# Kernel optimization log

Hardware: AMD Instinct MI355X
Metric: run time of the kernel (lower is better)

## Reference

```python
import jax, jax.numpy as jnp
import numpy as np

S = 1024      # seq_len
H = 768       # hidden_size
L = 50        # num_labels
E = 65536     # num_edges
SW = 10       # span_width


def setup_inputs() -> dict:
    key = jax.random.key(0)
    ks = jax.random.split(key, 10)
    hidden_states = jax.random.normal(ks[0], (1, S, H), jnp.float32)
    src = jax.random.randint(ks[1], (E,), 0, S)
    tgt = jax.random.randint(ks[2], (E,), 0, S)
    lbl = jax.random.randint(ks[3], (E,), 0, L)
    edges = jnp.stack([src, tgt, lbl], axis=-1)[None].astype(jnp.int32)  # [1,E,3]
    gcn_W = (jax.random.normal(ks[4], (L, H, H)) * 0.02).astype(jnp.float32)
    gcn_b = jnp.zeros((L, H), jnp.float32)
    attn_w = (jax.random.normal(ks[5], (H,)) * 0.02).astype(jnp.float32)
    attn_b = jnp.zeros((), jnp.float32)
    D = 3 * H
    ms_W1 = (jax.random.normal(ks[6], (D, D)) * 0.02).astype(jnp.float32)
    ms_b1 = jnp.zeros((D,), jnp.float32)
    ms_W2 = (jax.random.normal(ks[7], (D,)) * 0.02).astype(jnp.float32)
    ms_b2 = jnp.zeros((), jnp.float32)
    ant_W = (jax.random.normal(ks[8], (2 * D,)) * 0.02).astype(jnp.float32)
    ant_b = jnp.zeros((), jnp.float32)
    # candidate spans exactly as generate_candidate_spans with span_width=SW
    starts, ends = [], []
    for i in range(S):
        for j in range(i + 1, min(i + SW, S)):
            starts.append(i)
            ends.append(j)
    span_starts = jnp.asarray(np.array(starts, dtype=np.int32))
    span_ends = jnp.asarray(np.array(ends, dtype=np.int32))
    topk = int(S * 0.4)  # seq_lens*0.4 with all-ones attention mask
    return {
        'hidden_states': hidden_states, 'edges': edges,
        'gcn_W': gcn_W, 'gcn_b': gcn_b,
        'attn_w': attn_w, 'attn_b': attn_b,
        'ms_W1': ms_W1, 'ms_b1': ms_b1, 'ms_W2': ms_W2, 'ms_b2': ms_b2,
        'ant_W': ant_W, 'ant_b': ant_b,
        'span_starts': span_starts, 'span_ends': span_ends, 'topk': topk,
    }


def reference(hidden_states, edges, gcn_W, gcn_b, attn_w, attn_b,
              ms_W1, ms_b1, ms_W2, ms_b2, ant_W, ant_b,
              span_starts, span_ends, topk):
    B, Sq, Hd = hidden_states.shape  # B == 1
    nl = gcn_W.shape[0]
    x = hidden_states[0]  # [S,H]

    # ---- GCNLayer: per-label linear + scatter-add + degree norm + relu ----
    src = edges[0, :, 0]
    tgt = edges[0, :, 1]
    lbl = edges[0, :, 2]
    # aggregate source embeddings by (target,label): equivalent to applying
    # W_l per edge then index_add, since the transform is linear per label.
    seg = tgt * nl + lbl                               # [E]
    src_emb = x[src]                                   # [E,H]  gather
    agg = jax.ops.segment_sum(src_emb, seg, num_segments=Sq * nl)
    agg = agg.reshape(Sq, nl, Hd)                      # [S,L,H]
    cnt = jax.ops.segment_sum(jnp.ones_like(seg, jnp.float32), seg,
                              num_segments=Sq * nl).reshape(Sq, nl)
    out = jnp.einsum('slh,lhd->sd', agg, gcn_W) + cnt @ gcn_b  # [S,H]
    degree = jnp.clip(cnt.sum(axis=1), 1.0)[:, None]
    gcn_out = jax.nn.relu(out / degree)

    # combine_strategy == 'add'
    emb = x + gcn_out                                  # [S,H]

    # ---- SpanRepresentation: attention pooling over each span ----
    offs = jnp.arange(SW)                              # span length <= SW
    pos = span_starts[:, None] + offs                  # [N,SW]
    valid = pos <= span_ends[:, None]
    pos_c = jnp.minimum(pos, Sq - 1)
    win = emb[pos_c]                                   # [N,SW,H] gather
    scores = win @ attn_w + attn_b                     # [N,SW]
    scores = jnp.where(valid, scores, -1e9)
    aw = jax.nn.softmax(scores, axis=1)
    attn_out = jnp.einsum('nw,nwh->nh', aw, win)       # [N,H]
    span_vec = jnp.concatenate([emb[span_starts], emb[span_ends], attn_out],
                               axis=-1)                # [N,3H]

    # ---- MentionScorer ----
    hdn = jax.nn.relu(span_vec @ ms_W1 + ms_b1)
    mention_scores = hdn @ ms_W2 + ms_b2               # [N]

    # ---- prune_spans: top-k ----
    topk_scores, topk_idx = jax.lax.top_k(mention_scores, topk)
    pruned = span_vec[topk_idx]                        # [k,3H]

    # ---- antecedent scores: linear over concat pair == sum of two matvecs ----
    D = span_vec.shape[-1]
    s_i = pruned @ ant_W[:D]                           # [k]
    s_j = pruned @ ant_W[D:]                           # [k]
    ant_scores = s_i[:, None] + s_j[None, :] + ant_b   # [k,k]
    # triu mask (antecedent must strictly precede the mention)
    k = pruned.shape[0]
    triu = jnp.triu(jnp.ones((k, k), bool), k=0)
    ant_scores = jnp.where(triu, -1e4, ant_scores)
    dummy = jnp.zeros((k, 1), ant_scores.dtype)
    ant_scores_with_dummy = jnp.concatenate([dummy, ant_scores], axis=1)  # [k,k+1]
    return ant_scores_with_dummy
```

## Files before the change

kernel.cpp:

```cpp
#include <hip/hip_runtime.h>
#include <stdint.h>

typedef __attribute__((ext_vector_type(4))) float f32x4;
typedef __attribute__((ext_vector_type(4))) int i32x4;
typedef __attribute__((ext_vector_type(8))) int i32x8;

#define S_TOK 1024
#define H_DIM 768
#define NLBL  50
#define NEDGE 65536
#define NSEG  (S_TOK * NLBL)
#define NSPAN 9171
#define MPAD  9216
#define DDIM  2304
#define KTOP  409

__device__ __forceinline__ unsigned short f32_to_bf16u(float f) {
  unsigned u = __float_as_uint(f);
  u += 0x7fffu + ((u >> 16) & 1u);
  return (unsigned short)(u >> 16);
}
__device__ __forceinline__ float bf16u_to_f32(unsigned short h) {
  return __uint_as_float(((unsigned)h) << 16);
}
__device__ __forceinline__ unsigned short pack_fp8x2(float a, float b) {
  return (unsigned short)(__builtin_amdgcn_cvt_pk_fp8_f32(a, b, 0, false) & 0xffff);
}
__device__ __forceinline__ unsigned pack_fp8x4(float a, float b, float c, float d) {
  int v = __builtin_amdgcn_cvt_pk_fp8_f32(a, b, 0, false);
  v = __builtin_amdgcn_cvt_pk_fp8_f32(c, d, v, true);
  return (unsigned)v;
}
__device__ __forceinline__ unsigned char pack_fp8x1(float a) {
  return (unsigned char)(__builtin_amdgcn_cvt_pk_fp8_f32(a, a, 0, false) & 0xff);
}

__device__ __forceinline__ void gl_lds16(const void* g, void* l) {
  __builtin_amdgcn_global_load_lds((const __attribute__((address_space(1))) void*)g,
                                   (__attribute__((address_space(3))) void*)l, 16, 0, 0);
}

__global__ __launch_bounds__(256) void convert_fp8(
    const float* __restrict__ in, unsigned* __restrict__ out, int nquads) {
  int i = blockIdx.x * 256 + threadIdx.x;
  if (i >= nquads) return;
  float4 v = ((const float4*)in)[i];
  out[i] = pack_fp8x4(v.x, v.y, v.z, v.w);
}

__global__ __launch_bounds__(256) void transpose_fp8_b(
    const float* __restrict__ in, unsigned char* __restrict__ out, int R, int C) {
  __shared__ float tile[32][33];
  size_t boff = (size_t)blockIdx.z * R * C;
  int tx = threadIdx.x & 31, ty = threadIdx.x >> 5;
  int c0 = blockIdx.x * 32, r0 = blockIdx.y * 32;
#pragma unroll
  for (int i = 0; i < 4; i++)
    tile[ty + 8 * i][tx] = in[boff + (size_t)(r0 + ty + 8 * i) * C + c0 + tx];
  __syncthreads();
#pragma unroll
  for (int i = 0; i < 4; i++)
    out[boff + (size_t)(c0 + ty + 8 * i) * R + r0 + tx] = pack_fp8x1(tile[tx][ty + 8 * i]);
}

__global__ void edge_count2(const int* __restrict__ edges, int* __restrict__ seg_count,
                            int* __restrict__ tgt_count) {
  int e = blockIdx.x * 256 + threadIdx.x;
  if (e >= NEDGE) return;
  int tgt = edges[e * 3 + 1], lbl = edges[e * 3 + 2];
  atomicAdd(&seg_count[tgt * NLBL + lbl], 1);
  atomicAdd(&tgt_count[tgt], 1);
}

__global__ __launch_bounds__(1024) void scan_t(
    const int* __restrict__ cnt, int* __restrict__ offs) {
  __shared__ int part[1024];
  int t = threadIdx.x;
  int c = cnt[t];
  part[t] = c;
  __syncthreads();
  for (int o = 1; o < 1024; o <<= 1) {
    int v = part[t];
    int u = (t >= o) ? part[t - o] : 0;
    __syncthreads();
    part[t] = v + u;
    __syncthreads();
  }
  offs[t] = part[t] - c;
  if (t == 1023) offs[1024] = part[t];
}

__global__ void edge_scatter_t(const int* __restrict__ edges, const int* __restrict__ tgt_off,
                               int* __restrict__ cursor, int* __restrict__ sorted_row) {
  int e = blockIdx.x * 256 + threadIdx.x;
  if (e >= NEDGE) return;
  int src = edges[e * 3], tgt = edges[e * 3 + 1], lbl = edges[e * 3 + 2];
  int pos = tgt_off[tgt] + atomicAdd(&cursor[tgt], 1);
  sorted_row[pos] = lbl * S_TOK + src;
}

template <int EPI>
__global__ __launch_bounds__(256) void gemm_fp8(
    const unsigned char* __restrict__ A, const unsigned char* __restrict__ B,
    unsigned short* __restrict__ Y, float* __restrict__ C,
    const float* __restrict__ b1, const float* __restrict__ w2,
    int M, int Nn, int Kb, int mb, size_t strideB, size_t strideY) {
  __shared__ unsigned char As[128 * 128];
  __shared__ unsigned char Bs[128 * 128];
  int im = blockIdx.x % mb, in_ = blockIdx.x / mb;
  int m0 = im * 128, n0 = in_ * 128;
  const unsigned char* Bl = B + (size_t)blockIdx.y * strideB;

  int t = threadIdx.x;
  int wave = t >> 6, lane = t & 63;
  int wr = wave >> 1, wc = wave & 1;
  int quad = lane >> 4, l15 = lane & 15;
  int lrow = lane >> 3;
  int lk = ((lane & 7) ^ lrow) << 4;

  f32x4 acc[4][4];
  f32x4 zero = {0.f, 0.f, 0.f, 0.f};
#pragma unroll
  for (int mi = 0; mi < 4; mi++)
#pragma unroll
    for (int ni = 0; ni < 4; ni++) acc[mi][ni] = zero;

  for (int kt = 0; kt < Kb; kt += 128) {
#pragma unroll
    for (int i = 0; i < 4; i++) {
      int c = i * 4 + wave;
      int r = c * 8 + lrow;
      gl_lds16(A + (size_t)(m0 + r) * Kb + kt + lk, &As[c * 1024]);
      gl_lds16(Bl + (size_t)(n0 + r) * Kb + kt + lk, &Bs[c * 1024]);
    }
    __syncthreads();
    i32x8 af[4], bg[4];
#pragma unroll
    for (int mi = 0; mi < 4; mi++) {
      int r = wr * 64 + mi * 16 + l15;
      int base = r * 128;
      i32x4 lo = *(const i32x4*)&As[base + (((2 * quad) ^ (r & 7)) << 4)];
      i32x4 hi = *(const i32x4*)&As[base + (((2 * quad + 1) ^ (r & 7)) << 4)];
      af[mi] = __builtin_shufflevector(lo, hi, 0, 1, 2, 3, 4, 5, 6, 7);
    }
#pragma unroll
    for (int ni = 0; ni < 4; ni++) {
      int r = wc * 64 + ni * 16 + l15;
      int base = r * 128;
      i32x4 lo = *(const i32x4*)&Bs[base + (((2 * quad) ^ (r & 7)) << 4)];
      i32x4 hi = *(const i32x4*)&Bs[base + (((2 * quad + 1) ^ (r & 7)) << 4)];
      bg[ni] = __builtin_shufflevector(lo, hi, 0, 1, 2, 3, 4, 5, 6, 7);
    }
#pragma unroll
    for (int mi = 0; mi < 4; mi++)
#pragma unroll
      for (int ni = 0; ni < 4; ni++)
        acc[mi][ni] = __builtin_amdgcn_mfma_scale_f32_16x16x128_f8f6f4(
            af[mi], bg[ni], acc[mi][ni], 0, 0, 0, 0x7f7f7f7f, 0, 0x7f7f7f7f);
    __syncthreads();
  }

  if (EPI == 0) {
    unsigned short* Yl = Y + (size_t)blockIdx.y * strideY;
#pragma unroll
    for (int mi = 0; mi < 4; mi++) {
      int gm = m0 + wr * 64 + mi * 16 + quad * 4;
#pragma unroll
      for (int ni = 0; ni < 4; ni++) {
        int gn = n0 + wc * 64 + ni * 16 + l15;
#pragma unroll
        for (int r = 0; r < 4; r++)
          Yl[(size_t)(gm + r) * Nn + gn] = f32_to_bf16u(acc[mi][ni][r]);
      }
    }
  } else {
    float b1v[4], w2v[4];
#pragma unroll
    for (int ni = 0; ni < 4; ni++) {
      int gn = n0 + wc * 64 + ni * 16 + l15;
      b1v[ni] = b1[gn];
      w2v[ni] = w2[gn];
    }
#pragma unroll
    for (int mi = 0; mi < 4; mi++) {
      int gm = m0 + wr * 64 + mi * 16 + quad * 4;
      float part[4] = {0.f, 0.f, 0.f, 0.f};
#pragma unroll
      for (int ni = 0; ni < 4; ni++)
#pragma unroll
        for (int r = 0; r < 4; r++)
          part[r] += fmaxf(acc[mi][ni][r] + b1v[ni], 0.f) * w2v[ni];
#pragma unroll
      for (int o = 1; o < 16; o <<= 1)
#pragma unroll
        for (int r = 0; r < 4; r++) part[r] += __shfl_xor(part[r], o, 64);
      if (l15 == 0) {
#pragma unroll
        for (int r = 0; r < 4; r++)
          if (gm + r < M) atomicAdd(&C[gm + r], part[r]);
      }
    }
  }
}

__global__ __launch_bounds__(256) void gather_emb_kernel(
    const float* __restrict__ x, const unsigned short* __restrict__ Y,
    const int* __restrict__ tgt_off, const int* __restrict__ sorted_row,
    const int* __restrict__ seg_count, const float* __restrict__ gcn_b,
    float* __restrict__ emb) {
  int s = blockIdx.x;
  int t = threadIdx.x;
  int b = tgt_off[s], e = tgt_off[s + 1];
  float a0 = 0.f, a1 = 0.f, a2 = 0.f;
  int p = b;
  for (; p + 1 < e; p += 2) {
    const unsigned short* r0 = Y + (size_t)sorted_row[p] * H_DIM;
    const unsigned short* r1 = Y + (size_t)sorted_row[p + 1] * H_DIM;
    a0 += bf16u_to_f32(r0[t]) + bf16u_to_f32(r1[t]);
    a1 += bf16u_to_f32(r0[t + 256]) + bf16u_to_f32(r1[t + 256]);
    a2 += bf16u_to_f32(r0[t + 512]) + bf16u_to_f32(r1[t + 512]);
  }
  if (p < e) {
    const unsigned short* r0 = Y + (size_t)sorted_row[p] * H_DIM;
    a0 += bf16u_to_f32(r0[t]);
    a1 += bf16u_to_f32(r0[t + 256]);
    a2 += bf16u_to_f32(r0[t + 512]);
  }
  float deg = 0.f, b0 = 0.f, b1 = 0.f, b2 = 0.f;
#pragma unroll 5
  for (int l = 0; l < NLBL; l++) {
    float c = (float)seg_count[s * NLBL + l];
    deg += c;
    b0 += c * gcn_b[l * H_DIM + t];
    b1 += c * gcn_b[l * H_DIM + t + 256];
    b2 += c * gcn_b[l * H_DIM + t + 512];
  }
  float dinv = 1.f / fmaxf(deg, 1.f);
  emb[(size_t)s * H_DIM + t]       = x[(size_t)s * H_DIM + t]       + fmaxf((a0 + b0) * dinv, 0.f);
  emb[(size_t)s * H_DIM + t + 256] = x[(size_t)s * H_DIM + t + 256] + fmaxf((a1 + b1) * dinv, 0.f);
  emb[(size_t)s * H_DIM + t + 512] = x[(size_t)s * H_DIM + t + 512] + fmaxf((a2 + b2) * dinv, 0.f);
}

__global__ __launch_bounds__(256) void span_kernel(
    const float* __restrict__ emb, const float* __restrict__ attn_w,
    unsigned char* __restrict__ spanv) {
  int i = blockIdx.x;
  int nsp = 1023 - i; if (nsp > 9) nsp = 9;
  if (nsp <= 0) return;
  int nrow = nsp + 1;
  __shared__ float rows[10][768];
  __shared__ float dsh[10];
  int t = threadIdx.x;
  for (int idx = t; idx < nrow * 384; idx += 256) {
    int r = idx / 384, c2 = idx % 384;
    float2 v = ((const float2*)(emb + (size_t)(i + r) * H_DIM))[c2];
    rows[r][c2 * 2] = v.x; rows[r][c2 * 2 + 1] = v.y;
  }
  __syncthreads();
  int wave = t >> 6, lane = t & 63;
  for (int w = wave; w < nrow; w += 4) {
    float p = 0.f;
#pragma unroll
    for (int q = 0; q < 12; q++) p += rows[w][lane + 64 * q] * attn_w[lane + 64 * q];
#pragma unroll
    for (int o = 1; o < 64; o <<= 1) p += __shfl_xor(p, o, 64);
    if (lane == 0) dsh[w] = p;
  }
  __syncthreads();
  float d[10], ex[10];
  float mx = -1e30f;
  for (int w = 0; w < nrow; w++) { d[w] = dsh[w]; mx = fmaxf(mx, d[w]); }
  for (int w = 0; w < nrow; w++) ex[w] = __expf(d[w] - mx);
  bool has2 = (t < 128);
  float n00 = ex[0] * rows[0][2 * t], n01 = ex[0] * rows[0][2 * t + 1];
  float n10 = 0.f, n11 = 0.f;
  if (has2) { n10 = ex[0] * rows[0][2 * t + 512]; n11 = ex[0] * rows[0][2 * t + 513]; }
  float S = ex[0];
  int dd = i - 1014;
  int base = 9 * i - (dd > 0 ? dd * (dd - 1) / 2 : 0);
  unsigned short s0a = pack_fp8x2(rows[0][2 * t], rows[0][2 * t + 1]);
  unsigned short s0b = has2 ? pack_fp8x2(rows[0][2 * t + 512], rows[0][2 * t + 513]) : (unsigned short)0;
  for (int k = 1; k <= nsp; k++) {
    S += ex[k];
    n00 += ex[k] * rows[k][2 * t]; n01 += ex[k] * rows[k][2 * t + 1];
    if (has2) { n10 += ex[k] * rows[k][2 * t + 512]; n11 += ex[k] * rows[k][2 * t + 513]; }
    float inv = 1.f / S;
    unsigned short* out16 = (unsigned short*)(spanv + (size_t)(base + k - 1) * DDIM);
    out16[t] = s0a;
    out16[384 + t] = pack_fp8x2(rows[k][2 * t], rows[k][2 * t + 1]);
    out16[768 + t] = pack_fp8x2(n00 * inv, n01 * inv);
    if (has2) {
      out16[t + 256] = s0b;
      out16[384 + t + 256] = pack_fp8x2(rows[k][2 * t + 512], rows[k][2 * t + 513]);
      out16[768 + t + 256] = pack_fp8x2(n10 * inv, n11 * inv);
    }
  }
}

__device__ __forceinline__ unsigned score_key(float s) {
  unsigned b = __float_as_uint(s);
  return (b & 0x80000000u) ? ~b : (b | 0x80000000u);
}

__global__ __launch_bounds__(1024) void topk_kernel(
    const float* __restrict__ scores, int* __restrict__ topk_idx) {
  __shared__ unsigned skeys[NSPAN];
  __shared__ int hist[16 * 256];
  __shared__ int hsum[256];
  __shared__ unsigned sh_prefix;
  __shared__ int sh_remaining, sh_cnt;
  __shared__ unsigned long long keys[512];
  int t = threadIdx.x;
  int wv = t >> 6;
  for (int i = t; i < NSPAN; i += 1024) skeys[i] = score_key(scores[i]);
  unsigned prefix = 0;
  int remaining = KTOP;
  for (int p = 3; p >= 0; p--) {
    for (int b = t; b < 16 * 256; b += 1024) hist[b] = 0;
    __syncthreads();
    for (int i = t; i < NSPAN; i += 1024) {
      unsigned u = skeys[i];
      bool ok = (p == 3) ? true : ((u >> ((p + 1) * 8)) == prefix);
      if (ok) atomicAdd(&hist[wv * 256 + ((u >> (p * 8)) & 0xff)], 1);
    }
    __syncthreads();
    if (t < 256) {
      int s = 0;
#pragma unroll
      for (int w = 0; w < 16; w++) s += hist[w * 256 + t];
      hsum[t] = s;
    }
    __syncthreads();
    if (t == 0) {
      int rem = remaining;
      int b = 255;
      for (;; b--) {
        int c = hsum[b];
        if (c >= rem) break;
        rem -= c;
      }
      sh_prefix = (prefix << 8) | (unsigned)b;
      sh_remaining = rem;
    }
    __syncthreads();
    prefix = sh_prefix;
    remaining = sh_remaining;
    __syncthreads();
  }
  unsigned kth = prefix;
  if (t == 0) sh_cnt = 0;
  __syncthreads();
  for (int i = t; i < NSPAN; i += 1024) {
    unsigned u = skeys[i];
    if (u >= kth) {
      int pos = atomicAdd(&sh_cnt, 1);
      if (pos < 512) keys[pos] = (((unsigned long long)(~u)) << 32) | (unsigned)i;
    }
  }
  __syncthreads();
  int cnt = sh_cnt < 512 ? sh_cnt : 512;
  for (int i = t; i < 512; i += 1024)
    if (i >= cnt) keys[i] = ~0ull;
  __syncthreads();
  for (int ksz = 2; ksz <= 512; ksz <<= 1)
    for (int j = ksz >> 1; j > 0; j >>= 1) {
      if (t < 512) {
        int ixj = t ^ j;
        if (ixj > t) {
          unsigned long long a = keys[t], b = keys[ixj];
          bool up = ((t & ksz) == 0);
          if (up ? (a > b) : (a < b)) { keys[t] = b; keys[ixj] = a; }
        }
      }
      __syncthreads();
    }
  for (int i = t; i < KTOP; i += 1024) topk_idx[i] = (int)(keys[i] & 0xffffffffu);
}

__global__ __launch_bounds__(256) void sij_kernel(
    const unsigned char* __restrict__ spanv, const int* __restrict__ topk_idx,
    const float* __restrict__ antW, float* __restrict__ s_i, float* __restrict__ s_j) {
  int r = blockIdx.x;
  int idx = topk_idx[r];
  const unsigned* row32 = (const unsigned*)(spanv + (size_t)idx * DDIM);
  int t = threadIdx.x, lane = t & 63, wave = t >> 6;
  float pi = 0.f, pj = 0.f;
  for (int q = t; q < DDIM / 4; q += 256) {
    unsigned w = row32[q];
    float v0 = __builtin_amdgcn_cvt_f32_fp8(w, 0);
    float v1 = __builtin_amdgcn_cvt_f32_fp8(w, 1);
    float v2 = __builtin_amdgcn_cvt_f32_fp8(w, 2);
    float v3 = __builtin_amdgcn_cvt_f32_fp8(w, 3);
    const float* ai = antW + q * 4;
    const float* aj = antW + DDIM + q * 4;
    pi += v0 * ai[0] + v1 * ai[1] + v2 * ai[2] + v3 * ai[3];
    pj += v0 * aj[0] + v1 * aj[1] + v2 * aj[2] + v3 * aj[3];
  }
  for (int o = 32; o; o >>= 1) {
    pi += __shfl_down(pi, o, 64);
    pj += __shfl_down(pj, o, 64);
  }
  __shared__ float ri[4], rj[4];
  if (lane == 0) { ri[wave] = pi; rj[wave] = pj; }
  __syncthreads();
  if (t == 0) {
    s_i[r] = ri[0] + ri[1] + ri[2] + ri[3];
    s_j[r] = rj[0] + rj[1] + rj[2] + rj[3];
  }
}

__global__ void out_kernel(const float* __restrict__ s_i, const float* __restrict__ s_j,
                           const float* __restrict__ ant_b, float* __restrict__ out) {
  int idx = blockIdx.x * 256 + threadIdx.x;
  if (idx >= KTOP * (KTOP + 1)) return;
  int i = idx / (KTOP + 1), c = idx % (KTOP + 1);
  float v;
  if (c == 0) v = 0.f;
  else {
    int j = c - 1;
    v = (j >= i) ? -10000.f : (s_i[i] + s_j[j] + ant_b[0]);
  }
  out[idx] = v;
}

extern "C" void kernel_launch(void* const* d_in, const int* in_sizes, int n_in,
                              void* d_out, int out_size, void* d_ws, size_t ws_size,
                              hipStream_t stream) {
  const float* x      = (const float*)d_in[0];
  const int*   edges  = (const int*)d_in[1];
  const float* gcn_W  = (const float*)d_in[2];
  const float* gcn_b  = (const float*)d_in[3];
  const float* attn_w = (const float*)d_in[4];
  const float* ms_W1  = (const float*)d_in[6];
  const float* ms_b1  = (const float*)d_in[7];
  const float* ms_W2  = (const float*)d_in[8];
  const float* ant_W  = (const float*)d_in[10];
  const float* ant_b  = (const float*)d_in[11];

  size_t off = 0;
  char* wsb = (char*)d_ws;
  auto alloc = [&](size_t bytes) -> void* {
    void* p = wsb + off;
    off += (bytes + 255) & ~(size_t)255;
    return p;
  };
  unsigned short* Y    = (unsigned short*)alloc((size_t)NLBL * S_TOK * H_DIM * 2);
  unsigned char* WtB   = (unsigned char*)alloc((size_t)NLBL * H_DIM * H_DIM);
  unsigned char* Wt2   = (unsigned char*)alloc((size_t)DDIM * DDIM);
  unsigned char* spanv = (unsigned char*)alloc((size_t)MPAD * DDIM);
  unsigned char* Xb    = (unsigned char*)alloc((size_t)S_TOK * H_DIM);
  int* seg_count  = (int*)alloc(NSEG * 4);
  int* tgt_count  = (int*)alloc(S_TOK * 4);
  int* cursor     = (int*)alloc(S_TOK * 4);
  float* scores   = (float*)alloc(MPAD * 4);
  size_t zero_bytes = (char*)(scores + MPAD) - (char*)seg_count;
  int* tgt_off    = (int*)alloc((S_TOK + 4) * 4);
  int* sorted_row = (int*)alloc(NEDGE * 4);
  float* emb    = (float*)alloc((size_t)S_TOK * H_DIM * 4);
  int* topk_idx = (int*)alloc(512 * 4);
  float* s_i    = (float*)alloc(512 * 4);
  float* s_j    = (float*)alloc(512 * 4);
  (void)ws_size; (void)in_sizes; (void)n_in; (void)out_size;

  hipMemsetAsync(seg_count, 0, zero_bytes, stream);

  dim3 b256(256);
  convert_fp8<<<(S_TOK * H_DIM / 4 + 255) / 256, b256, 0, stream>>>(x, (unsigned*)Xb,
                                                                    S_TOK * H_DIM / 4);
  transpose_fp8_b<<<dim3(H_DIM / 32, H_DIM / 32, NLBL), b256, 0, stream>>>(gcn_W, WtB, H_DIM, H_DIM);
  transpose_fp8_b<<<dim3(DDIM / 32, DDIM / 32, 1), b256, 0, stream>>>(ms_W1, Wt2, DDIM, DDIM);
  edge_count2<<<NEDGE / 256, b256, 0, stream>>>(edges, seg_count, tgt_count);
  scan_t<<<1, 1024, 0, stream>>>(tgt_count, tgt_off);
  edge_scatter_t<<<NEDGE / 256, b256, 0, stream>>>(edges, tgt_off, cursor, sorted_row);
  gemm_fp8<0><<<dim3(48, NLBL), b256, 0, stream>>>(
      Xb, WtB, Y, nullptr, nullptr, nullptr,
      S_TOK, H_DIM, H_DIM, 8, (size_t)H_DIM * H_DIM, (size_t)S_TOK * H_DIM);
  gather_emb_kernel<<<S_TOK, b256, 0, stream>>>(x, Y, tgt_off, sorted_row, seg_count, gcn_b, emb);
  span_kernel<<<S_TOK, b256, 0, stream>>>(emb, attn_w, spanv);
  gemm_fp8<1><<<dim3(72 * 18, 1), b256, 0, stream>>>(
      spanv, Wt2, nullptr, scores, ms_b1, ms_W2,
      NSPAN, DDIM, DDIM, 72, 0, 0);
  topk_kernel<<<1, 1024, 0, stream>>>(scores, topk_idx);
  sij_kernel<<<KTOP, b256, 0, stream>>>(spanv, topk_idx, ant_W, s_i, s_j);
  out_kernel<<<(KTOP * (KTOP + 1) + 255) / 256, b256, 0, stream>>>(s_i, s_j, ant_b, (float*)d_out);
}
```

Baseline: 450.6 us.

## Aggregate neighbors before GCN matmul and use one flattened split-K GEMM

Reorders the GCN step so neighbor features are summed per (target, label) first, into an FP8 [S, L*H] matrix. A single split-K FP8 GEMM against the flattened transposed weights then produces the output, with atomic fp32 accumulation. This removes the per-label [L,S,H] bf16 intermediate and its write and gather traffic. The cost is a serial per-target aggregation kernel with an in-block rank sort, atomics in the GEMM epilogue, an extra buffer to zero, and FP8 rounding of the aggregated sums, which can be larger in magnitude than the raw inputs.

```diff
diff --git a/kernel.cpp b/kernel.cpp
--- a/kernel.cpp
+++ b/kernel.cpp
@@ -14,6 +14,7 @@
 #define MPAD  9216
 #define DDIM  2304
 #define KTOP  409
+#define KFLAT (NLBL * H_DIM)
 
 __device__ __forceinline__ unsigned short f32_to_bf16u(float f) {
   unsigned u = __float_as_uint(f);
@@ -38,14 +39,6 @@
 __device__ __forceinline__ void gl_lds16(const void* g, void* l) {
   __builtin_amdgcn_global_load_lds((const __attribute__((address_space(1))) void*)g,
                                    (__attribute__((address_space(3))) void*)l, 16, 0, 0);
-}
-
-__global__ __launch_bounds__(256) void convert_fp8(
-    const float* __restrict__ in, unsigned* __restrict__ out, int nquads) {
-  int i = blockIdx.x * 256 + threadIdx.x;
-  if (i >= nquads) return;
-  float4 v = ((const float4*)in)[i];
-  out[i] = pack_fp8x4(v.x, v.y, v.z, v.w);
 }
 
 __global__ __launch_bounds__(256) void transpose_fp8_b(
@@ -61,6 +54,25 @@
 #pragma unroll
   for (int i = 0; i < 4; i++)
     out[boff + (size_t)(c0 + ty + 8 * i) * R + r0 + tx] = pack_fp8x1(tile[tx][ty + 8 * i]);
+}
+
+__global__ __launch_bounds__(256) void transpose_fp8_flat(
+    const float* __restrict__ in, unsigned char* __restrict__ out) {
+  __shared__ float tile[32][33];
+  int l = blockIdx.z;
+  const float* inl = in + (size_t)l * H_DIM * H_DIM;
+  int tx = threadIdx.x & 31, ty = threadIdx.x >> 5;
+  int c0 = blockIdx.x * 32;
+  int r0 = blockIdx.y * 32;
+#pragma unroll
+  for (int i = 0; i < 4; i++)
+    tile[ty + 8 * i][tx] = inl[(size_t)(r0 + ty + 8 * i) * H_DIM + c0 + tx];
+  __syncthreads();
+#pragma unroll
+  for (int i = 0; i < 4; i++) {
+    int d = c0 + ty + 8 * i, h = r0 + tx;
+    out[(size_t)d * KFLAT + l * H_DIM + h] = pack_fp8x1(tile[tx][ty + 8 * i]);
+  }
 }
 
 __global__ void edge_count2(const int* __restrict__ edges, int* __restrict__ seg_count,
@@ -99,17 +111,58 @@
   sorted_row[pos] = lbl * S_TOK + src;
 }
 
+__global__ __launch_bounds__(256) void agg_kernel(
+    const float* __restrict__ x, const int* __restrict__ tgt_off,
+    const int* __restrict__ sorted_row, unsigned char* __restrict__ agg) {
+  int s = blockIdx.x, t = threadIdx.x;
+  int b = tgt_off[s], e = tgt_off[s + 1];
+  int n = e - b;
+  __shared__ int ed[256], eds[256];
+  __shared__ float row[768];
+  for (int i = t; i < n; i += 256) ed[i] = sorted_row[b + i];
+  __syncthreads();
+  if (t < n) {
+    int v = ed[t], rank = 0;
+    for (int i = 0; i < n; i++) {
+      int u = ed[i];
+      rank += (u < v) || (u == v && i < t);
+    }
+    eds[rank] = v;
+  }
+  __syncthreads();
+  unsigned char* arow = agg + (size_t)s * KFLAT;
+  int p = 0;
+  for (int l = 0; l < NLBL; l++) {
+    float a0 = 0.f, a1 = 0.f, a2 = 0.f;
+    while (p < n) {
+      int v = eds[p];
+      if ((v >> 10) != l) break;
+      const float* xr = x + (size_t)(v & 1023) * H_DIM;
+      a0 += xr[t]; a1 += xr[t + 256]; a2 += xr[t + 512];
+      p++;
+    }
+    row[t] = a0; row[t + 256] = a1; row[t + 512] = a2;
+    __syncthreads();
+    if (t < 192) {
+      unsigned w = pack_fp8x4(row[4 * t], row[4 * t + 1], row[4 * t + 2], row[4 * t + 3]);
+      ((unsigned*)(arow + l * H_DIM))[t] = w;
+    }
+    __syncthreads();
+  }
+}
+
 template <int EPI>
 __global__ __launch_bounds__(256) void gemm_fp8(
     const unsigned char* __restrict__ A, const unsigned char* __restrict__ B,
     unsigned short* __restrict__ Y, float* __restrict__ C,
     const float* __restrict__ b1, const float* __restrict__ w2,
-    int M, int Nn, int Kb, int mb, size_t strideB, size_t strideY) {
+    int M, int Nn, int Kb, int Klen, int mb, size_t strideB, size_t strideY) {
   __shared__ unsigned char As[128 * 128];
   __shared__ unsigned char Bs[128 * 128];
   int im = blockIdx.x % mb, in_ = blockIdx.x / mb;
   int m0 = im * 128, n0 = in_ * 128;
   const unsigned char* Bl = B + (size_t)blockIdx.y * strideB;
+  int kbase = (EPI == 2) ? blockIdx.y * Klen : 0;
 
   int t = threadIdx.x;
   int wave = t >> 6, lane = t & 63;
@@ -125,7 +178,7 @@
 #pragma unroll
     for (int ni = 0; ni < 4; ni++) acc[mi][ni] = zero;
 
-  for (int kt = 0; kt < Kb; kt += 128) {
+  for (int kt = kbase; kt < kbase + Klen; kt += 128) {
 #pragma unroll
     for (int i = 0; i < 4; i++) {
       int c = i * 4 + wave;
@@ -173,7 +226,7 @@
           Yl[(size_t)(gm + r) * Nn + gn] = f32_to_bf16u(acc[mi][ni][r]);
       }
     }
-  } else {
+  } else if (EPI == 1) {
     float b1v[4], w2v[4];
 #pragma unroll
     for (int ni = 0; ni < 4; ni++) {
@@ -200,32 +253,26 @@
           if (gm + r < M) atomicAdd(&C[gm + r], part[r]);
       }
     }
-  }
-}
-
-__global__ __launch_bounds__(256) void gather_emb_kernel(
-    const float* __restrict__ x, const unsigned short* __restrict__ Y,
-    const int* __restrict__ tgt_off, const int* __restrict__ sorted_row,
+  } else {
+#pragma unroll
+    for (int mi = 0; mi < 4; mi++) {
+      int gm = m0 + wr * 64 + mi * 16 + quad * 4;
+#pragma unroll
+      for (int ni = 0; ni < 4; ni++) {
+        int gn = n0 + wc * 64 + ni * 16 + l15;
+#pragma unroll
+        for (int r = 0; r < 4; r++)
+          atomicAdd(&C[(size_t)(gm + r) * Nn + gn], acc[mi][ni][r]);
+      }
+    }
+  }
+}
+
+__global__ __launch_bounds__(256) void finalize_emb(
+    const float* __restrict__ x, const float* __restrict__ out2,
     const int* __restrict__ seg_count, const float* __restrict__ gcn_b,
     float* __restrict__ emb) {
-  int s = blockIdx.x;
-  int t = threadIdx.x;
-  int b = tgt_off[s], e = tgt_off[s + 1];
-  float a0 = 0.f, a1 = 0.f, a2 = 0.f;
-  int p = b;
-  for (; p + 1 < e; p += 2) {
-    const unsigned short* r0 = Y + (size_t)sorted_row[p] * H_DIM;
-    const unsigned short* r1 = Y + (size_t)sorted_row[p + 1] * H_DIM;
-    a0 += bf16u_to_f32(r0[t]) + bf16u_to_f32(r1[t]);
-    a1 += bf16u_to_f32(r0[t + 256]) + bf16u_to_f32(r1[t + 256]);
-    a2 += bf16u_to_f32(r0[t + 512]) + bf16u_to_f32(r1[t + 512]);
-  }
-  if (p < e) {
-    const unsigned short* r0 = Y + (size_t)sorted_row[p] * H_DIM;
-    a0 += bf16u_to_f32(r0[t]);
-    a1 += bf16u_to_f32(r0[t + 256]);
-    a2 += bf16u_to_f32(r0[t + 512]);
-  }
+  int s = blockIdx.x, t = threadIdx.x;
   float deg = 0.f, b0 = 0.f, b1 = 0.f, b2 = 0.f;
 #pragma unroll 5
   for (int l = 0; l < NLBL; l++) {
@@ -236,9 +283,10 @@
     b2 += c * gcn_b[l * H_DIM + t + 512];
   }
   float dinv = 1.f / fmaxf(deg, 1.f);
-  emb[(size_t)s * H_DIM + t]       = x[(size_t)s * H_DIM + t]       + fmaxf((a0 + b0) * dinv, 0.f);
-  emb[(size_t)s * H_DIM + t + 256] = x[(size_t)s * H_DIM + t + 256] + fmaxf((a1 + b1) * dinv, 0.f);
-  emb[(size_t)s * H_DIM + t + 512] = x[(size_t)s * H_DIM + t + 512] + fmaxf((a2 + b2) * dinv, 0.f);
+  const float* o = out2 + (size_t)s * H_DIM;
+  emb[(size_t)s * H_DIM + t]       = x[(size_t)s * H_DIM + t]       + fmaxf((o[t] + b0) * dinv, 0.f);
+  emb[(size_t)s * H_DIM + t + 256] = x[(size_t)s * H_DIM + t + 256] + fmaxf((o[t + 256] + b1) * dinv, 0.f);
+  emb[(size_t)s * H_DIM + t + 512] = x[(size_t)s * H_DIM + t + 512] + fmaxf((o[t + 512] + b2) * dinv, 0.f);
 }
 
 __global__ __launch_bounds__(256) void span_kernel(
@@ -444,16 +492,16 @@
     off += (bytes + 255) & ~(size_t)255;
     return p;
   };
-  unsigned short* Y    = (unsigned short*)alloc((size_t)NLBL * S_TOK * H_DIM * 2);
-  unsigned char* WtB   = (unsigned char*)alloc((size_t)NLBL * H_DIM * H_DIM);
+  unsigned char* WtF   = (unsigned char*)alloc((size_t)H_DIM * KFLAT);
+  unsigned char* agg   = (unsigned char*)alloc((size_t)S_TOK * KFLAT);
   unsigned char* Wt2   = (unsigned char*)alloc((size_t)DDIM * DDIM);
   unsigned char* spanv = (unsigned char*)alloc((size_t)MPAD * DDIM);
-  unsigned char* Xb    = (unsigned char*)alloc((size_t)S_TOK * H_DIM);
   int* seg_count  = (int*)alloc(NSEG * 4);
   int* tgt_count  = (int*)alloc(S_TOK * 4);
   int* cursor     = (int*)alloc(S_TOK * 4);
   float* scores   = (float*)alloc(MPAD * 4);
-  size_t zero_bytes = (char*)(scores + MPAD) - (char*)seg_count;
+  float* out2     = (float*)alloc((size_t)S_TOK * H_DIM * 4);
+  size_t zero_bytes = (char*)(out2 + (size_t)S_TOK * H_DIM) - (char*)seg_count;
   int* tgt_off    = (int*)alloc((S_TOK + 4) * 4);
   int* sorted_row = (int*)alloc(NEDGE * 4);
   float* emb    = (float*)alloc((size_t)S_TOK * H_DIM * 4);
@@ -465,21 +513,20 @@
   hipMemsetAsync(seg_count, 0, zero_bytes, stream);
 
   dim3 b256(256);
-  convert_fp8<<<(S_TOK * H_DIM / 4 + 255) / 256, b256, 0, stream>>>(x, (unsigned*)Xb,
-                                                                    S_TOK * H_DIM / 4);
-  transpose_fp8_b<<<dim3(H_DIM / 32, H_DIM / 32, NLBL), b256, 0, stream>>>(gcn_W, WtB, H_DIM, H_DIM);
+  transpose_fp8_flat<<<dim3(H_DIM / 32, H_DIM / 32, NLBL), b256, 0, stream>>>(gcn_W, WtF);
   transpose_fp8_b<<<dim3(DDIM / 32, DDIM / 32, 1), b256, 0, stream>>>(ms_W1, Wt2, DDIM, DDIM);
   edge_count2<<<NEDGE / 256, b256, 0, stream>>>(edges, seg_count, tgt_count);
   scan_t<<<1, 1024, 0, stream>>>(tgt_count, tgt_off);
   edge_scatter_t<<<NEDGE / 256, b256, 0, stream>>>(edges, tgt_off, cursor, sorted_row);
-  gemm_fp8<0><<<dim3(48, NLBL), b256, 0, stream>>>(
-      Xb, WtB, Y, nullptr, nullptr, nullptr,
-      S_TOK, H_DIM, H_DIM, 8, (size_t)H_DIM * H_DIM, (size_t)S_TOK * H_DIM);
-  gather_emb_kernel<<<S_TOK, b256, 0, stream>>>(x, Y, tgt_off, sorted_row, seg_count, gcn_b, emb);
+  agg_kernel<<<S_TOK, b256, 0, stream>>>(x, tgt_off, sorted_row, agg);
+  gemm_fp8<2><<<dim3(48, 12), b256, 0, stream>>>(
+      agg, WtF, nullptr, out2, nullptr, nullptr,
+      S_TOK, H_DIM, KFLAT, KFLAT / 12, 8, 0, 0);
+  finalize_emb<<<S_TOK, b256, 0, stream>>>(x, out2, seg_count, gcn_b, emb);
   span_kernel<<<S_TOK, b256, 0, stream>>>(emb, attn_w, spanv);
   gemm_fp8<1><<<dim3(72 * 18, 1), b256, 0, stream>>>(
       spanv, Wt2, nullptr, scores, ms_b1, ms_W2,
-      NSPAN, DDIM, DDIM, 72, 0, 0);
+      NSPAN, DDIM, DDIM, DDIM, 72, 0, 0);
   topk_kernel<<<1, 1024, 0, stream>>>(scores, topk_idx);
   sij_kernel<<<KTOP, b256, 0, stream>>>(spanv, topk_idx, ant_W, s_i, s_j);
   out_kernel<<<(KTOP * (KTOP + 1) + 255) / 256, b256, 0, stream>>>(s_i, s_j, ant_b, (float*)d_out);
```

Measured after the change: 479.7 us. 6.5% more time.

## Store per-label GCN outputs as fp8 with LDS-staged coalesced writes

Applied to the files above, without the earlier changes.

The per-label GEMM output Y is now written in fp8 instead of bf16, which halves the 50x1024x768 intermediate. The epilogue stages the tile through shared memory so global stores become 16-byte vectors instead of scattered 2-byte writes. The gather kernel now reads 4 fp8 values per thread with 192 threads and uses float4 for the bias, x and emb accesses. The cost is extra precision loss in the aggregated GCN messages, which could push results past tolerance.

```diff
diff --git a/kernel.cpp b/kernel.cpp
--- a/kernel.cpp
+++ b/kernel.cpp
@@ -102,7 +102,7 @@
 template <int EPI>
 __global__ __launch_bounds__(256) void gemm_fp8(
     const unsigned char* __restrict__ A, const unsigned char* __restrict__ B,
-    unsigned short* __restrict__ Y, float* __restrict__ C,
+    unsigned char* __restrict__ Y, float* __restrict__ C,
     const float* __restrict__ b1, const float* __restrict__ w2,
     int M, int Nn, int Kb, int mb, size_t strideB, size_t strideY) {
   __shared__ unsigned char As[128 * 128];
@@ -161,17 +161,21 @@
   }
 
   if (EPI == 0) {
-    unsigned short* Yl = Y + (size_t)blockIdx.y * strideY;
-#pragma unroll
-    for (int mi = 0; mi < 4; mi++) {
-      int gm = m0 + wr * 64 + mi * 16 + quad * 4;
-#pragma unroll
-      for (int ni = 0; ni < 4; ni++) {
-        int gn = n0 + wc * 64 + ni * 16 + l15;
+    unsigned char* Yl = Y + (size_t)blockIdx.y * strideY;
+#pragma unroll
+    for (int mi = 0; mi < 4; mi++)
+#pragma unroll
+      for (int ni = 0; ni < 4; ni++)
 #pragma unroll
         for (int r = 0; r < 4; r++)
-          Yl[(size_t)(gm + r) * Nn + gn] = f32_to_bf16u(acc[mi][ni][r]);
-      }
+          As[(wr * 64 + mi * 16 + quad * 4 + r) * 128 + wc * 64 + ni * 16 + l15] =
+              pack_fp8x1(acc[mi][ni][r]);
+    __syncthreads();
+#pragma unroll
+    for (int i = 0; i < 4; i++) {
+      int idx = t + i * 256;
+      int row = idx >> 3, off2 = (idx & 7) << 4;
+      *(i32x4*)(Yl + (size_t)(m0 + row) * Nn + n0 + off2) = *(const i32x4*)&As[row * 128 + off2];
     }
   } else {
     float b1v[4], w2v[4];
@@ -203,42 +207,48 @@
   }
 }
 
-__global__ __launch_bounds__(256) void gather_emb_kernel(
-    const float* __restrict__ x, const unsigned short* __restrict__ Y,
+__global__ __launch_bounds__(192) void gather_emb_kernel(
+    const float* __restrict__ x, const unsigned char* __restrict__ Y,
     const int* __restrict__ tgt_off, const int* __restrict__ sorted_row,
     const int* __restrict__ seg_count, const float* __restrict__ gcn_b,
     float* __restrict__ emb) {
   int s = blockIdx.x;
   int t = threadIdx.x;
   int b = tgt_off[s], e = tgt_off[s + 1];
-  float a0 = 0.f, a1 = 0.f, a2 = 0.f;
+  float a0 = 0.f, a1 = 0.f, a2 = 0.f, a3 = 0.f;
   int p = b;
   for (; p + 1 < e; p += 2) {
-    const unsigned short* r0 = Y + (size_t)sorted_row[p] * H_DIM;
-    const unsigned short* r1 = Y + (size_t)sorted_row[p + 1] * H_DIM;
-    a0 += bf16u_to_f32(r0[t]) + bf16u_to_f32(r1[t]);
-    a1 += bf16u_to_f32(r0[t + 256]) + bf16u_to_f32(r1[t + 256]);
-    a2 += bf16u_to_f32(r0[t + 512]) + bf16u_to_f32(r1[t + 512]);
+    const unsigned* r0 = (const unsigned*)(Y + (size_t)sorted_row[p] * H_DIM);
+    const unsigned* r1 = (const unsigned*)(Y + (size_t)sorted_row[p + 1] * H_DIM);
+    unsigned w0 = r0[t], w1 = r1[t];
+    a0 += __builtin_amdgcn_cvt_f32_fp8(w0, 0) + __builtin_amdgcn_cvt_f32_fp8(w1, 0);
+    a1 += __builtin_amdgcn_cvt_f32_fp8(w0, 1) + __builtin_amdgcn_cvt_f32_fp8(w1, 1);
+    a2 += __builtin_amdgcn_cvt_f32_fp8(w0, 2) + __builtin_amdgcn_cvt_f32_fp8(w1, 2);
+    a3 += __builtin_amdgcn_cvt_f32_fp8(w0, 3) + __builtin_amdgcn_cvt_f32_fp8(w1, 3);
   }
   if (p < e) {
-    const unsigned short* r0 = Y + (size_t)sorted_row[p] * H_DIM;
-    a0 += bf16u_to_f32(r0[t]);
-    a1 += bf16u_to_f32(r0[t + 256]);
-    a2 += bf16u_to_f32(r0[t + 512]);
-  }
-  float deg = 0.f, b0 = 0.f, b1 = 0.f, b2 = 0.f;
+    unsigned w0 = ((const unsigned*)(Y + (size_t)sorted_row[p] * H_DIM))[t];
+    a0 += __builtin_amdgcn_cvt_f32_fp8(w0, 0);
+    a1 += __builtin_amdgcn_cvt_f32_fp8(w0, 1);
+    a2 += __builtin_amdgcn_cvt_f32_fp8(w0, 2);
+    a3 += __builtin_amdgcn_cvt_f32_fp8(w0, 3);
+  }
+  float deg = 0.f, b0 = 0.f, b1 = 0.f, b2 = 0.f, b3 = 0.f;
 #pragma unroll 5
   for (int l = 0; l < NLBL; l++) {
     float c = (float)seg_count[s * NLBL + l];
     deg += c;
-    b0 += c * gcn_b[l * H_DIM + t];
-    b1 += c * gcn_b[l * H_DIM + t + 256];
-    b2 += c * gcn_b[l * H_DIM + t + 512];
+    float4 g = ((const float4*)(gcn_b + l * H_DIM))[t];
+    b0 += c * g.x; b1 += c * g.y; b2 += c * g.z; b3 += c * g.w;
   }
   float dinv = 1.f / fmaxf(deg, 1.f);
-  emb[(size_t)s * H_DIM + t]       = x[(size_t)s * H_DIM + t]       + fmaxf((a0 + b0) * dinv, 0.f);
-  emb[(size_t)s * H_DIM + t + 256] = x[(size_t)s * H_DIM + t + 256] + fmaxf((a1 + b1) * dinv, 0.f);
-  emb[(size_t)s * H_DIM + t + 512] = x[(size_t)s * H_DIM + t + 512] + fmaxf((a2 + b2) * dinv, 0.f);
+  float4 xe = ((const float4*)(x + (size_t)s * H_DIM))[t];
+  float4 o;
+  o.x = xe.x + fmaxf((a0 + b0) * dinv, 0.f);
+  o.y = xe.y + fmaxf((a1 + b1) * dinv, 0.f);
+  o.z = xe.z + fmaxf((a2 + b2) * dinv, 0.f);
+  o.w = xe.w + fmaxf((a3 + b3) * dinv, 0.f);
+  ((float4*)(emb + (size_t)s * H_DIM))[t] = o;
 }
 
 __global__ __launch_bounds__(256) void span_kernel(
@@ -444,7 +454,7 @@
     off += (bytes + 255) & ~(size_t)255;
     return p;
   };
-  unsigned short* Y    = (unsigned short*)alloc((size_t)NLBL * S_TOK * H_DIM * 2);
+  unsigned char* Y     = (unsigned char*)alloc((size_t)NLBL * S_TOK * H_DIM);
   unsigned char* WtB   = (unsigned char*)alloc((size_t)NLBL * H_DIM * H_DIM);
   unsigned char* Wt2   = (unsigned char*)alloc((size_t)DDIM * DDIM);
   unsigned char* spanv = (unsigned char*)alloc((size_t)MPAD * DDIM);
@@ -475,7 +485,7 @@
   gemm_fp8<0><<<dim3(48, NLBL), b256, 0, stream>>>(
       Xb, WtB, Y, nullptr, nullptr, nullptr,
       S_TOK, H_DIM, H_DIM, 8, (size_t)H_DIM * H_DIM, (size_t)S_TOK * H_DIM);
-  gather_emb_kernel<<<S_TOK, b256, 0, stream>>>(x, Y, tgt_off, sorted_row, seg_count, gcn_b, emb);
+  gather_emb_kernel<<<S_TOK, dim3(192), 0, stream>>>(x, Y, tgt_off, sorted_row, seg_count, gcn_b, emb);
   span_kernel<<<S_TOK, b256, 0, stream>>>(emb, attn_w, spanv);
   gemm_fp8<1><<<dim3(72 * 18, 1), b256, 0, stream>>>(
       spanv, Wt2, nullptr, scores, ms_b1, ms_W2,
```

Result: no change. 451.5 us (+0.2%).
